# Kernel optimization log

Hardware: AMD Instinct MI355X
Metric: run time of the kernel (lower is better)

Reference implementation:

```python
import jax, jax.numpy as jnp
import numpy as np

NEG_SLOPE = 0.01  # torch leaky_relu default

def _lrelu(x):
    return jax.nn.leaky_relu(x, NEG_SLOPE)

def _l2norm(x, axis):
    # torch F.normalize(p=2, eps=1e-12)
    n = jnp.linalg.norm(x, axis=axis, keepdims=True)
    return x / jnp.maximum(n, 1e-12)

def setup_inputs() -> dict:
    key = jax.random.key(0)
    ks = jax.random.split(key, 12)
    Nda, Nq, C, Din, Dout = 10000, 64, 1024, 128, 256
    target_adj = (jax.random.uniform(ks[0], (Nda, Nda)) < 0.002).astype(jnp.float32)
    query_adj = (jax.random.uniform(ks[1], (Nq, Nq)) < 0.2).astype(jnp.float32)
    node_features_da = jax.random.normal(ks[2], (Nda, Din), dtype=jnp.float32)
    node_features_q = jax.random.normal(ks[3], (Nq, Din), dtype=jnp.float32)
    candidate_set = jax.random.randint(ks[4], (C,), 0, Nda)
    candidate_adj = (jax.random.uniform(ks[5], (C, C)) < 0.01).astype(jnp.float32)
    s_in = 1.0 / np.sqrt(Din).astype(np.float32)
    s_out = 1.0 / np.sqrt(Dout).astype(np.float32)
    W1_da = jax.random.normal(ks[6], (Din, Dout), dtype=jnp.float32) * s_in
    W1_q = jax.random.normal(ks[7], (Din, Dout), dtype=jnp.float32) * s_in
    W2_da = jax.random.normal(ks[8], (Dout, Dout), dtype=jnp.float32) * s_out
    W2_q = jax.random.normal(ks[9], (Dout, Dout), dtype=jnp.float32) * s_out
    threshold = jnp.float32(0.2)
    return {"target_adj": target_adj, "node_features_da": node_features_da,
            "query_adj": query_adj, "node_features_q": node_features_q,
            "candidate_set": candidate_set, "candidate_adj": candidate_adj,
            "threshold": threshold, "W1_da": W1_da, "W1_q": W1_q,
            "W2_da": W2_da, "W2_q": W2_q}

def _cross_cosine(q, da, candidate_set):
    # cosine similarity between each query node and each candidate target node: [Nq, C]
    return _l2norm(q, 1) @ _l2norm(da[candidate_set], 1).T

def reference(target_adj, node_features_da, query_adj, node_features_q,
              candidate_set, candidate_adj, threshold, W1_da, W1_q, W2_da, W2_q):
    # layer 1: GCN propagation on both graphs (gcn(adj,x) = adj @ x @ W)
    da1 = _lrelu(target_adj @ (node_features_da @ W1_da))   # [Nda, D]
    q1 = _lrelu(query_adj @ (node_features_q @ W1_q))       # [Nq, D]
    c1 = _cross_cosine(q1, da1, candidate_set)               # [Nq, C]
    pre_da1 = da1[candidate_set]                             # [C, D]
    # NOTE: da1[candidate_set].data = ... mutates a temporary in torch -> no-op on da1
    att_da1 = _lrelu(da1)                                    # dropout in eval = identity
    h1_q = c1 @ pre_da1                                      # [Nq, D]
    att_q1 = _lrelu(q1 + _l2norm(h1_q, 0))
    # layer 2
    da2 = _lrelu(target_adj @ (att_da1 @ W2_da))
    q2 = _lrelu(query_adj @ (att_q1 @ W2_q))
    c2 = _cross_cosine(q2, da2, candidate_set)
    pre_da2 = da2[candidate_set]
    att_da2 = _lrelu(da2)                                    # in-place update is again a no-op
    h2_q = c2 @ pre_da2
    att_q2 = _lrelu(q2 + _l2norm(h2_q, 0))
    # graph-level matching score per target node
    emb = jnp.mean(att_q2, axis=0, keepdims=True)            # [1, D]
    num = att_da2 @ emb[0]                                   # [Nda]
    den = jnp.maximum(jnp.linalg.norm(att_da2, axis=1) * jnp.linalg.norm(emb), 1e-8)
    end = (num / den)[None, :]                               # [1, Nda]
    # threshold selection expressed with a mask (jit-safe, same math: excluded
    # rows/cols are zero and do not affect L2 norms, sums, or the trace)
    m = (end[0] > threshold).astype(att_da2.dtype)           # [Nda]
    F_ = att_da2 * m[:, None]
    re_adj = F_ @ F_.T                                       # [Nda, Nda]
    nor_re = _l2norm(re_adj, 1) * target_adj                 # elementwise with original adj
    cnt = jnp.sum(m)
    total = jnp.sum(nor_re)
    tr = jnp.trace(nor_re)
    has = cnt > 0
    pre_avg_degree = jnp.where(has, total / jnp.maximum(cnt, 1.0), 0.0)
    pre_avg_nodes = jnp.where(has, tr, 0.0)
    pre_density = jnp.where(has, 2.0 * total / (tr * (tr - 1.0) + 1e-4), 0.0)
    return (end, att_da2, att_q2, pre_avg_degree, pre_density, pre_avg_nodes)
```

## Files before the change

kernel.cpp:

```cpp
#include <hip/hip_runtime.h>

constexpr int NDA = 10000;
constexpr int NQ  = 64;
constexpr int CND = 1024;
constexpr int DIN = 128;
constexpr int D   = 256;
constexpr int CAP = 96;

#define LRELU(x) ((x) >= 0.f ? (x) : 0.01f * (x))

__device__ __forceinline__ float wave_red64(float v) {
#pragma unroll
    for (int o = 32; o; o >>= 1) v += __shfl_down(v, o);
    return v;
}

__global__ __launch_bounds__(256) void build_csr(const float* __restrict__ adj,
                                                 int* __restrict__ cols,
                                                 int* __restrict__ rowcnt) {
    int row = blockIdx.x;
    __shared__ int scnt;
    if (threadIdx.x == 0) scnt = 0;
    __syncthreads();
    const float4* rp = (const float4*)(adj + (size_t)row * NDA);
    for (int i = threadIdx.x; i < NDA / 4; i += 256) {
        float4 v = rp[i];
        if (v.x != 0.f) { int s = atomicAdd(&scnt, 1); if (s < CAP) cols[row * CAP + s] = 4 * i; }
        if (v.y != 0.f) { int s = atomicAdd(&scnt, 1); if (s < CAP) cols[row * CAP + s] = 4 * i + 1; }
        if (v.z != 0.f) { int s = atomicAdd(&scnt, 1); if (s < CAP) cols[row * CAP + s] = 4 * i + 2; }
        if (v.w != 0.f) { int s = atomicAdd(&scnt, 1); if (s < CAP) cols[row * CAP + s] = 4 * i + 3; }
    }
    __syncthreads();
    if (threadIdx.x == 0) rowcnt[row] = min(scnt, CAP);
}

template <int W, bool RELU_IN>
__global__ void spmm(const int* __restrict__ cols,
                     const int* __restrict__ rowcnt,
                     const float* __restrict__ X,
                     float* __restrict__ out) {
    int row = blockIdx.x;
    int d = threadIdx.x;
    int cnt = rowcnt[row];
    __shared__ int sc[CAP];
    if (d < CAP && d < cnt) sc[d] = cols[row * CAP + d];
    __syncthreads();
    float a0 = 0.f, a1 = 0.f, a2 = 0.f, a3 = 0.f;
    int k = 0;
    for (; k + 4 <= cnt; k += 4) {
        float v0 = X[(size_t)sc[k + 0] * W + d];
        float v1 = X[(size_t)sc[k + 1] * W + d];
        float v2 = X[(size_t)sc[k + 2] * W + d];
        float v3 = X[(size_t)sc[k + 3] * W + d];
        if (RELU_IN) { v0 = LRELU(v0); v1 = LRELU(v1); v2 = LRELU(v2); v3 = LRELU(v3); }
        a0 += v0; a1 += v1; a2 += v2; a3 += v3;
    }
    for (; k < cnt; k++) {
        float v = X[(size_t)sc[k] * W + d];
        if (RELU_IN) v = LRELU(v);
        a0 += v;
    }
    out[(size_t)row * W + d] = (a0 + a1) + (a2 + a3);
}

template <bool RELU_C, bool DUAL>
__global__ __launch_bounds__(256) void gemm64(const float* __restrict__ A,
                                              const float* __restrict__ B,
                                              float* __restrict__ C,
                                              float* __restrict__ C2,
                                              int M, int N, int K) {
    __shared__ float As[16][68];
    __shared__ float Bs[16][68];
    const int bm = blockIdx.x * 64;
    const int bn = blockIdx.y * 64;
    const int tid = threadIdx.x;
    const int tx = tid & 15, ty = tid >> 4;
    float acc[4][4] = {};
    for (int k0 = 0; k0 < K; k0 += 16) {
        {
            int m = tid >> 2;
            int k4 = (tid & 3) * 4;
            float4 v = make_float4(0.f, 0.f, 0.f, 0.f);
            if (bm + m < M) v = *(const float4*)(A + (size_t)(bm + m) * K + k0 + k4);
            As[k4 + 0][m] = v.x; As[k4 + 1][m] = v.y; As[k4 + 2][m] = v.z; As[k4 + 3][m] = v.w;
        }
        {
            int kk = tid >> 4;
            int n4 = (tid & 15) * 4;
            float4 v = *(const float4*)(B + (size_t)(k0 + kk) * N + bn + n4);
            Bs[kk][n4 + 0] = v.x; Bs[kk][n4 + 1] = v.y; Bs[kk][n4 + 2] = v.z; Bs[kk][n4 + 3] = v.w;
        }
        __syncthreads();
#pragma unroll
        for (int kk = 0; kk < 16; kk++) {
            float av[4], bv[4];
#pragma unroll
            for (int i = 0; i < 4; i++) av[i] = As[kk][ty * 4 + i];
#pragma unroll
            for (int j = 0; j < 4; j++) bv[j] = Bs[kk][tx * 4 + j];
#pragma unroll
            for (int i = 0; i < 4; i++)
#pragma unroll
                for (int j = 0; j < 4; j++) acc[i][j] += av[i] * bv[j];
        }
        __syncthreads();
    }
#pragma unroll
    for (int i = 0; i < 4; i++) {
        int r = bm + ty * 4 + i;
        if (r < M) {
            float4 v;
            v.x = acc[i][0]; v.y = acc[i][1]; v.z = acc[i][2]; v.w = acc[i][3];
            if (RELU_C) { v.x = LRELU(v.x); v.y = LRELU(v.y); v.z = LRELU(v.z); v.w = LRELU(v.w); }
            *(float4*)(C + (size_t)r * N + bn + tx * 4) = v;
            if (DUAL) {
                float4 u;
                u.x = LRELU(v.x); u.y = LRELU(v.y); u.z = LRELU(v.z); u.w = LRELU(v.w);
                *(float4*)(C2 + (size_t)r * N + bn + tx * 4) = u;
            }
        }
    }
}

__global__ __launch_bounds__(256) void qpath_kernel(const float* __restrict__ Fq,
                                                    const float* __restrict__ Wq,
                                                    const float* __restrict__ Qadj,
                                                    float* __restrict__ q_out,
                                                    float* __restrict__ rnqsq,
                                                    int K) {
    __shared__ float As[16][68];
    __shared__ float Bs[16][68];
    __shared__ float Xs[64][68];
    __shared__ float Qs[64][68];
    __shared__ float sq[64];
    const int bn = blockIdx.x * 64;
    const int tid = threadIdx.x;
    const int tx = tid & 15, ty = tid >> 4;
    float acc[4][4] = {};
    for (int k0 = 0; k0 < K; k0 += 16) {
        {
            int m = tid >> 2;
            int k4 = (tid & 3) * 4;
            float4 v = *(const float4*)(Fq + (size_t)m * K + k0 + k4);
            As[k4 + 0][m] = v.x; As[k4 + 1][m] = v.y; As[k4 + 2][m] = v.z; As[k4 + 3][m] = v.w;
        }
        {
            int kk = tid >> 4;
            int n4 = (tid & 15) * 4;
            float4 v = *(const float4*)(Wq + (size_t)(k0 + kk) * D + bn + n4);
            Bs[kk][n4 + 0] = v.x; Bs[kk][n4 + 1] = v.y; Bs[kk][n4 + 2] = v.z; Bs[kk][n4 + 3] = v.w;
        }
        __syncthreads();
#pragma unroll
        for (int kk = 0; kk < 16; kk++) {
            float av[4], bv[4];
#pragma unroll
            for (int i = 0; i < 4; i++) av[i] = As[kk][ty * 4 + i];
#pragma unroll
            for (int j = 0; j < 4; j++) bv[j] = Bs[kk][tx * 4 + j];
#pragma unroll
            for (int i = 0; i < 4; i++)
#pragma unroll
                for (int j = 0; j < 4; j++) acc[i][j] += av[i] * bv[j];
        }
        __syncthreads();
    }
#pragma unroll
    for (int i = 0; i < 4; i++)
#pragma unroll
        for (int j = 0; j < 4; j++) Xs[ty * 4 + i][tx * 4 + j] = acc[i][j];
    for (int l = tid; l < NQ * NQ; l += 256) Qs[l >> 6][l & 63] = Qadj[l];
    if (tid < 64) sq[tid] = 0.f;
    __syncthreads();
    float a2[4][4] = {};
#pragma unroll 4
    for (int kk = 0; kk < NQ; kk++) {
        float av[4], bv[4];
#pragma unroll
        for (int i = 0; i < 4; i++) av[i] = Qs[ty * 4 + i][kk];
#pragma unroll
        for (int j = 0; j < 4; j++) bv[j] = Xs[kk][tx * 4 + j];
#pragma unroll
        for (int i = 0; i < 4; i++)
#pragma unroll
            for (int j = 0; j < 4; j++) a2[i][j] += av[i] * bv[j];
    }
#pragma unroll
    for (int i = 0; i < 4; i++) {
        float rp = 0.f;
#pragma unroll
        for (int j = 0; j < 4; j++) {
            float v = LRELU(a2[i][j]);
            q_out[(ty * 4 + i) * D + bn + tx * 4 + j] = v;
            rp += v * v;
        }
        atomicAdd(&sq[ty * 4 + i], rp);
    }
    __syncthreads();
    if (tid < 64) atomicAdd(&rnqsq[tid], sq[tid]);
}

__global__ __launch_bounds__(256) void candnorms_kernel(const float* __restrict__ da,
                                                        const int* __restrict__ cand,
                                                        float* __restrict__ rncinv) {
    int b = blockIdx.x;
    const float* src = da + (size_t)cand[b] * D;
    float v = src[threadIdx.x];
    float p = wave_red64(v * v);
    __shared__ float red[4];
    int w = threadIdx.x >> 6, lane = threadIdx.x & 63;
    if (lane == 0) red[w] = p;
    __syncthreads();
    if (threadIdx.x == 0)
        rncinv[b] = 1.f / fmaxf(sqrtf(red[0] + red[1] + red[2] + red[3]), 1e-12f);
}

constexpr int CCH = 128;
__global__ __launch_bounds__(256) void candM_split(const float* __restrict__ da,
                                                   const int* __restrict__ cand,
                                                   const float* __restrict__ rncinv,
                                                   float* __restrict__ M) {
    __shared__ float SA[8][64], SB[8][64];
    const int ti = blockIdx.x, tj = blockIdx.y;
    const int cb = blockIdx.z * CCH;
    const int tid = threadIdx.x;
    const int tx = tid & 15, ty = tid >> 4;
    float acc[4][4] = {};
    for (int c0 = 0; c0 < CCH; c0 += 8) {
        for (int l = tid; l < 512; l += 256) {
            int rr = l >> 6, c = l & 63;
            int cr = cand[cb + c0 + rr];
            float s = rncinv[cb + c0 + rr];
            SA[rr][c] = da[(size_t)cr * D + ti * 64 + c] * s;
            SB[rr][c] = da[(size_t)cr * D + tj * 64 + c];
        }
        __syncthreads();
#pragma unroll
        for (int rr = 0; rr < 8; rr++) {
            float av[4], bv[4];
#pragma unroll
            for (int i = 0; i < 4; i++) av[i] = SA[rr][ty * 4 + i];
#pragma unroll
            for (int j = 0; j < 4; j++) bv[j] = SB[rr][tx * 4 + j];
#pragma unroll
            for (int i = 0; i < 4; i++)
#pragma unroll
                for (int j = 0; j < 4; j++) acc[i][j] += av[i] * bv[j];
        }
        __syncthreads();
    }
#pragma unroll
    for (int i = 0; i < 4; i++)
#pragma unroll
        for (int j = 0; j < 4; j++)
            atomicAdd(&M[(ti * 64 + ty * 4 + i) * D + tj * 64 + tx * 4 + j], acc[i][j]);
}

__global__ __launch_bounds__(256) void hq_gemm(const float* __restrict__ q,
                                               const float* __restrict__ rnqsq,
                                               float* __restrict__ M,
                                               float* __restrict__ h) {
    __shared__ float As[16][68];
    __shared__ float Bs[16][68];
    const int bn = blockIdx.x * 64;
    const int tid = threadIdx.x;
    const int tx = tid & 15, ty = tid >> 4;
    float acc[4][4] = {};
    const float4 z4 = make_float4(0.f, 0.f, 0.f, 0.f);
    for (int k0 = 0; k0 < D; k0 += 16) {
        {
            int m = tid >> 2;
            int k4 = (tid & 3) * 4;
            float s = 1.f / fmaxf(sqrtf(rnqsq[m]), 1e-12f);
            float4 v = *(const float4*)(q + (size_t)m * D + k0 + k4);
            As[k4 + 0][m] = v.x * s; As[k4 + 1][m] = v.y * s;
            As[k4 + 2][m] = v.z * s; As[k4 + 3][m] = v.w * s;
        }
        {
            int kk = tid >> 4;
            int n4 = (tid & 15) * 4;
            float4 v = *(const float4*)(M + (size_t)(k0 + kk) * D + bn + n4);
            *(float4*)(M + (size_t)(k0 + kk) * D + bn + n4) = z4;
            Bs[kk][n4 + 0] = v.x; Bs[kk][n4 + 1] = v.y; Bs[kk][n4 + 2] = v.z; Bs[kk][n4 + 3] = v.w;
        }
        __syncthreads();
#pragma unroll
        for (int kk = 0; kk < 16; kk++) {
            float av[4], bv[4];
#pragma unroll
            for (int i = 0; i < 4; i++) av[i] = As[kk][ty * 4 + i];
#pragma unroll
            for (int j = 0; j < 4; j++) bv[j] = Bs[kk][tx * 4 + j];
#pragma unroll
            for (int i = 0; i < 4; i++)
#pragma unroll
                for (int j = 0; j < 4; j++) acc[i][j] += av[i] * bv[j];
        }
        __syncthreads();
    }
#pragma unroll
    for (int i = 0; i < 4; i++)
#pragma unroll
        for (int j = 0; j < 4; j++)
            h[(ty * 4 + i) * D + bn + tx * 4 + j] = acc[i][j];
}

__global__ __launch_bounds__(256) void attq_kernel(const float* __restrict__ q,
                                                   const float* __restrict__ h,
                                                   float* __restrict__ attq,
                                                   float* __restrict__ emb,
                                                   float* __restrict__ rnqsq) {
    int d = threadIdx.x;
    if (d < 64) rnqsq[d] = 0.f;
    float hv[NQ];
    float ss = 0.f;
#pragma unroll
    for (int r = 0; r < NQ; r++) {
        hv[r] = h[r * D + d];
        ss += hv[r] * hv[r];
    }
    float inv = 1.f / fmaxf(sqrtf(ss), 1e-12f);
    float es = 0.f;
#pragma unroll
    for (int r = 0; r < NQ; r++) {
        float v = q[r * D + d] + hv[r] * inv;
        v = LRELU(v);
        attq[r * D + d] = v;
        es += v;
    }
    if (emb) {
        float e = es * (1.f / (float)NQ);
        emb[d] = e;
        float p = wave_red64(e * e);
        __shared__ float red[4];
        int w = d >> 6, lane = d & 63;
        if (lane == 0) red[w] = p;
        __syncthreads();
        if (d == 0) emb[D] = sqrtf(red[0] + red[1] + red[2] + red[3]);
    }
}

__global__ __launch_bounds__(256) void end_kernel(const float* __restrict__ A,
                                                  const float* __restrict__ emb,
                                                  const float* __restrict__ thr_p,
                                                  float* __restrict__ endv,
                                                  float* __restrict__ m,
                                                  float* __restrict__ cnt) {
    __shared__ float se[D];
    __shared__ float scnt;
    int d = threadIdx.x;
    se[d] = emb[d];
    if (d == 0) scnt = 0.f;
    __syncthreads();
    float embn = emb[D];
    float thr = *thr_p;
    int w = d >> 6, lane = d & 63;
    int row = blockIdx.x * 4 + w;
    const float* ar = A + (size_t)row * D;
    float num = 0.f, sq = 0.f;
#pragma unroll
    for (int s = 0; s < 4; s++) {
        float v = ar[lane + 64 * s];
        num += v * se[lane + 64 * s];
        sq += v * v;
    }
#pragma unroll
    for (int o = 32; o; o >>= 1) { num += __shfl_down(num, o); sq += __shfl_down(sq, o); }
    if (lane == 0) {
        float den = fmaxf(sqrtf(sq) * embn, 1e-8f);
        float e = num / den;
        endv[row] = e;
        float mv = e > thr ? 1.f : 0.f;
        m[row] = mv;
        if (mv != 0.f) atomicAdd(&scnt, 1.f);
    }
    __syncthreads();
    if (d == 0 && scnt != 0.f) atomicAdd(cnt, scnt);
}

constexpr int GCHUNK = 1000;
__global__ __launch_bounds__(256) void G_kernel(const float* __restrict__ A,
                                                const float* __restrict__ m,
                                                float* __restrict__ G) {
    __shared__ float SA[8][64], SB[8][64];
    int ti = blockIdx.x >> 2, tj = blockIdx.x & 3;
    int base = blockIdx.y * GCHUNK;
    int tid = threadIdx.x;
    int tx = tid & 15, ty = tid >> 4;
    float acc[4][4] = {};
    for (int g0 = 0; g0 < GCHUNK; g0 += 8) {
        for (int l = tid; l < 512; l += 256) {
            int rr = l >> 6, c = l & 63;
            int r = base + g0 + rr;
            float mv = m[r];
            SA[rr][c] = A[(size_t)r * D + ti * 64 + c] * mv;
            SB[rr][c] = A[(size_t)r * D + tj * 64 + c];
        }
        __syncthreads();
#pragma unroll
        for (int rr = 0; rr < 8; rr++) {
            float av[4], bv[4];
#pragma unroll
            for (int i = 0; i < 4; i++) av[i] = SA[rr][ty * 4 + i];
#pragma unroll
            for (int j = 0; j < 4; j++) bv[j] = SB[rr][tx * 4 + j];
#pragma unroll
            for (int i = 0; i < 4; i++)
#pragma unroll
                for (int j = 0; j < 4; j++) acc[i][j] += av[i] * bv[j];
        }
        __syncthreads();
    }
#pragma unroll
    for (int i = 0; i < 4; i++)
#pragma unroll
        for (int j = 0; j < 4; j++)
            atomicAdd(&G[(ti * 64 + ty * 4 + i) * D + tj * 64 + tx * 4 + j], acc[i][j]);
}

__global__ __launch_bounds__(256) void final_kernel(const int* __restrict__ cols,
                                                    const int* __restrict__ rowcnt,
                                                    const float* __restrict__ m,
                                                    const float* __restrict__ A,
                                                    const float* __restrict__ H,
                                                    double* __restrict__ total,
                                                    double* __restrict__ tr) {
    int i = blockIdx.x;
    if (m[i] == 0.f) return;
    __shared__ float sa[D];
    __shared__ int sc[CAP];
    __shared__ float red[4], red2[4];
    __shared__ float sdenom;
    int d = threadIdx.x;
    float av = A[(size_t)i * D + d];
    sa[d] = av;
    int cnt = rowcnt[i];
    if (d < cnt) sc[d] = cols[i * CAP + d];
    float p = wave_red64(av * H[(size_t)i * D + d]);
    int w = d >> 6, lane = d & 63;
    if (lane == 0) red[w] = p;
    __syncthreads();
    if (d == 0) sdenom = fmaxf(sqrtf(red[0] + red[1] + red[2] + red[3]), 1e-12f);
    __syncthreads();
    float accs = 0.f, acct = 0.f;
    for (int k = w; k < cnt; k += 4) {
        int j = sc[k];
        if (m[j] != 0.f) {
            const float* aj = A + (size_t)j * D;
            float t = sa[lane] * aj[lane] + sa[lane + 64] * aj[lane + 64]
                    + sa[lane + 128] * aj[lane + 128] + sa[lane + 192] * aj[lane + 192];
            t = wave_red64(t);
            if (lane == 0) { accs += t; if (j == i) acct += t; }
        }
    }
    if (lane == 0) { red[w] = accs; red2[w] = acct; }
    __syncthreads();
    if (d == 0) {
        float s = red[0] + red[1] + red[2] + red[3];
        float t2 = red2[0] + red2[1] + red2[2] + red2[3];
        double inv = 1.0 / (double)sdenom;
        if (s != 0.f) atomicAdd(total, (double)s * inv);
        if (t2 != 0.f) atomicAdd(tr, (double)t2 * inv);
    }
}

__global__ void scalars_kernel(const float* __restrict__ cnt,
                               const double* __restrict__ total,
                               const double* __restrict__ tr,
                               float* __restrict__ out) {
    float c = *cnt;
    float T = (float)*total;
    float R = (float)*tr;
    bool has = c > 0.f;
    out[0] = has ? (T / fmaxf(c, 1.f)) : 0.f;
    out[1] = has ? (2.f * T / (R * (R - 1.f) + 1e-4f)) : 0.f;
    out[2] = has ? R : 0.f;
}

extern "C" void kernel_launch(void* const* d_in, const int* in_sizes, int n_in,
                              void* d_out, int out_size, void* d_ws, size_t ws_size,
                              hipStream_t stream) {
    (void)in_sizes; (void)n_in; (void)out_size; (void)ws_size;
    const float* adj  = (const float*)d_in[0];
    const float* Fda  = (const float*)d_in[1];
    const float* Qadj = (const float*)d_in[2];
    const float* Fq   = (const float*)d_in[3];
    const int*   cand = (const int*)d_in[4];
    const float* thr  = (const float*)d_in[6];
    const float* W1da = (const float*)d_in[7];
    const float* W1q  = (const float*)d_in[8];
    const float* W2da = (const float*)d_in[9];
    const float* W2q  = (const float*)d_in[10];

    float* out = (float*)d_out;
    float* o_end    = out;
    float* o_attda2 = out + NDA;
    float* o_attq2  = out + NDA + (size_t)NDA * D;
    float* o_sc     = o_attq2 + NQ * D;

    char* w = (char*)d_ws;
    size_t off = 0;
    auto alloc = [&](size_t b) { size_t r = off; off += (b + 255) & ~(size_t)255; return r; };
    float* bufA = (float*)(w + alloc((size_t)NDA * D * 4));
    float* bufB = (float*)(w + alloc((size_t)NDA * D * 4));
    float* bufC = (float*)(w + alloc((size_t)NDA * D * 4));
    int* colsb   = (int*)(w + alloc((size_t)NDA * CAP * 4));
    int* rowcntb = (int*)(w + alloc((size_t)NDA * 4));
    float* mbuf  = (float*)(w + alloc((size_t)NDA * 4));
    char* zbase = w + alloc(525000);
    float* Gb     = (float*)zbase;
    float* Mb     = (float*)(zbase + 262144);
    float* rnqsqb = (float*)(zbase + 524288);
    float* cntb   = (float*)(zbase + 524544);
    double* totb  = (double*)(zbase + 524552);
    double* trb   = (double*)(zbase + 524560);
    float* q1b  = (float*)(w + alloc((size_t)NQ * D * 4));
    float* aq1  = (float*)(w + alloc((size_t)NQ * D * 4));
    float* q2b  = (float*)(w + alloc((size_t)NQ * D * 4));
    float* hb   = (float*)(w + alloc((size_t)NQ * D * 4));
    float* rncinv = (float*)(w + alloc((size_t)CND * 4));
    float* embb   = (float*)(w + alloc((size_t)(D + 1) * 4));

    hipMemsetAsync(zbase, 0, 524576, stream);

    const dim3 gBig((NDA + 63) / 64, D / 64);

    build_csr<<<NDA, 256, 0, stream>>>(adj, colsb, rowcntb);
    qpath_kernel<<<D / 64, 256, 0, stream>>>(Fq, W1q, Qadj, q1b, rnqsqb, DIN);
    spmm<DIN, false><<<NDA, DIN, 0, stream>>>(colsb, rowcntb, Fda, bufA);
    gemm64<true, false><<<gBig, 256, 0, stream>>>(bufA, W1da, bufB, nullptr, NDA, D, DIN);
    candnorms_kernel<<<CND, 256, 0, stream>>>(bufB, cand, rncinv);
    candM_split<<<dim3(4, 4, CND / CCH), 256, 0, stream>>>(bufB, cand, rncinv, Mb);
    hq_gemm<<<D / 64, 256, 0, stream>>>(q1b, rnqsqb, Mb, hb);
    attq_kernel<<<1, 256, 0, stream>>>(q1b, hb, aq1, nullptr, rnqsqb);
    qpath_kernel<<<D / 64, 256, 0, stream>>>(aq1, W2q, Qadj, q2b, rnqsqb, D);
    spmm<D, true><<<NDA, D, 0, stream>>>(colsb, rowcntb, bufB, bufA);
    gemm64<true, true><<<gBig, 256, 0, stream>>>(bufA, W2da, bufC, o_attda2, NDA, D, D);
    candnorms_kernel<<<CND, 256, 0, stream>>>(bufC, cand, rncinv);
    candM_split<<<dim3(4, 4, CND / CCH), 256, 0, stream>>>(bufC, cand, rncinv, Mb);
    hq_gemm<<<D / 64, 256, 0, stream>>>(q2b, rnqsqb, Mb, hb);
    attq_kernel<<<1, 256, 0, stream>>>(q2b, hb, o_attq2, embb, rnqsqb);
    end_kernel<<<NDA / 4, 256, 0, stream>>>(o_attda2, embb, thr, o_end, mbuf, cntb);
    G_kernel<<<dim3(16, NDA / GCHUNK), 256, 0, stream>>>(o_attda2, mbuf, Gb);
    gemm64<false, false><<<gBig, 256, 0, stream>>>(o_attda2, Gb, bufB, nullptr, NDA, D, D);
    final_kernel<<<NDA, 256, 0, stream>>>(colsb, rowcntb, mbuf, o_attda2, bufB, totb, trb);
    scalars_kernel<<<1, 1, 0, stream>>>(cntb, totb, trb, o_sc);
}
```

Before: 1.080 ms.

## Fuse row norms into GEMM epilogue, merge hq/attq, gather bf16 activations in SpMM

Row squared norms are now accumulated with atomics in the GEMM epilogue, which replaces the separate candidate-norm kernels. The hq GEMM and attq kernels are merged into one multi-block kernel, and the embedding-norm computation moves into end_kernel. The first-layer activated output is also written in bf16, so the second SpMM gathers half the bytes. The cost is extra atomics per row and reduced precision in the layer-2 input, which could move results past tolerance.

```diff
diff --git a/kernel.cpp b/kernel.cpp
--- a/kernel.cpp
+++ b/kernel.cpp
@@ -1,4 +1,5 @@
 #include <hip/hip_runtime.h>
+#include <hip/hip_bf16.h>
 
 constexpr int NDA = 10000;
 constexpr int NQ  = 64;
@@ -8,6 +9,8 @@
 constexpr int CAP = 96;
 
 #define LRELU(x) ((x) >= 0.f ? (x) : 0.01f * (x))
+
+struct alignas(8) bf4 { __hip_bfloat16 a, b, c, d; };
 
 __device__ __forceinline__ float wave_red64(float v) {
 #pragma unroll
@@ -34,11 +37,11 @@
     if (threadIdx.x == 0) rowcnt[row] = min(scnt, CAP);
 }
 
-template <int W, bool RELU_IN>
-__global__ void spmm(const int* __restrict__ cols,
-                     const int* __restrict__ rowcnt,
-                     const float* __restrict__ X,
-                     float* __restrict__ out) {
+template <int W>
+__global__ void spmm_f32(const int* __restrict__ cols,
+                         const int* __restrict__ rowcnt,
+                         const float* __restrict__ X,
+                         float* __restrict__ out) {
     int row = blockIdx.x;
     int d = threadIdx.x;
     int cnt = rowcnt[row];
@@ -48,26 +51,44 @@
     float a0 = 0.f, a1 = 0.f, a2 = 0.f, a3 = 0.f;
     int k = 0;
     for (; k + 4 <= cnt; k += 4) {
-        float v0 = X[(size_t)sc[k + 0] * W + d];
-        float v1 = X[(size_t)sc[k + 1] * W + d];
-        float v2 = X[(size_t)sc[k + 2] * W + d];
-        float v3 = X[(size_t)sc[k + 3] * W + d];
-        if (RELU_IN) { v0 = LRELU(v0); v1 = LRELU(v1); v2 = LRELU(v2); v3 = LRELU(v3); }
-        a0 += v0; a1 += v1; a2 += v2; a3 += v3;
-    }
-    for (; k < cnt; k++) {
-        float v = X[(size_t)sc[k] * W + d];
-        if (RELU_IN) v = LRELU(v);
-        a0 += v;
-    }
+        a0 += X[(size_t)sc[k + 0] * W + d];
+        a1 += X[(size_t)sc[k + 1] * W + d];
+        a2 += X[(size_t)sc[k + 2] * W + d];
+        a3 += X[(size_t)sc[k + 3] * W + d];
+    }
+    for (; k < cnt; k++) a0 += X[(size_t)sc[k] * W + d];
     out[(size_t)row * W + d] = (a0 + a1) + (a2 + a3);
 }
 
-template <bool RELU_C, bool DUAL>
+__global__ void spmm_bf16(const int* __restrict__ cols,
+                          const int* __restrict__ rowcnt,
+                          const __hip_bfloat16* __restrict__ X,
+                          float* __restrict__ out) {
+    int row = blockIdx.x;
+    int d = threadIdx.x;
+    int cnt = rowcnt[row];
+    __shared__ int sc[CAP];
+    if (d < CAP && d < cnt) sc[d] = cols[row * CAP + d];
+    __syncthreads();
+    float a0 = 0.f, a1 = 0.f, a2 = 0.f, a3 = 0.f;
+    int k = 0;
+    for (; k + 4 <= cnt; k += 4) {
+        a0 += __bfloat162float(X[(size_t)sc[k + 0] * D + d]);
+        a1 += __bfloat162float(X[(size_t)sc[k + 1] * D + d]);
+        a2 += __bfloat162float(X[(size_t)sc[k + 2] * D + d]);
+        a3 += __bfloat162float(X[(size_t)sc[k + 3] * D + d]);
+    }
+    for (; k < cnt; k++) a0 += __bfloat162float(X[(size_t)sc[k] * D + d]);
+    out[(size_t)row * D + d] = (a0 + a1) + (a2 + a3);
+}
+
+template <bool RELU_C, bool DUAL, bool BF16OUT>
 __global__ __launch_bounds__(256) void gemm64(const float* __restrict__ A,
                                               const float* __restrict__ B,
                                               float* __restrict__ C,
                                               float* __restrict__ C2,
+                                              __hip_bfloat16* __restrict__ bfout,
+                                              float* __restrict__ rowsq,
                                               int M, int N, int K) {
     __shared__ float As[16][68];
     __shared__ float Bs[16][68];
@@ -113,10 +134,22 @@
             v.x = acc[i][0]; v.y = acc[i][1]; v.z = acc[i][2]; v.w = acc[i][3];
             if (RELU_C) { v.x = LRELU(v.x); v.y = LRELU(v.y); v.z = LRELU(v.z); v.w = LRELU(v.w); }
             *(float4*)(C + (size_t)r * N + bn + tx * 4) = v;
+            if (rowsq) {
+                float rp = v.x * v.x + v.y * v.y + v.z * v.z + v.w * v.w;
+                atomicAdd(&rowsq[r], rp);
+            }
             if (DUAL) {
                 float4 u;
                 u.x = LRELU(v.x); u.y = LRELU(v.y); u.z = LRELU(v.z); u.w = LRELU(v.w);
                 *(float4*)(C2 + (size_t)r * N + bn + tx * 4) = u;
+            }
+            if (BF16OUT) {
+                bf4 t;
+                t.a = __float2bfloat16(LRELU(v.x));
+                t.b = __float2bfloat16(LRELU(v.y));
+                t.c = __float2bfloat16(LRELU(v.z));
+                t.d = __float2bfloat16(LRELU(v.w));
+                *(bf4*)(bfout + (size_t)r * N + bn + tx * 4) = t;
             }
         }
     }
@@ -200,25 +233,10 @@
     if (tid < 64) atomicAdd(&rnqsq[tid], sq[tid]);
 }
 
-__global__ __launch_bounds__(256) void candnorms_kernel(const float* __restrict__ da,
-                                                        const int* __restrict__ cand,
-                                                        float* __restrict__ rncinv) {
-    int b = blockIdx.x;
-    const float* src = da + (size_t)cand[b] * D;
-    float v = src[threadIdx.x];
-    float p = wave_red64(v * v);
-    __shared__ float red[4];
-    int w = threadIdx.x >> 6, lane = threadIdx.x & 63;
-    if (lane == 0) red[w] = p;
-    __syncthreads();
-    if (threadIdx.x == 0)
-        rncinv[b] = 1.f / fmaxf(sqrtf(red[0] + red[1] + red[2] + red[3]), 1e-12f);
-}
-
 constexpr int CCH = 128;
 __global__ __launch_bounds__(256) void candM_split(const float* __restrict__ da,
                                                    const int* __restrict__ cand,
-                                                   const float* __restrict__ rncinv,
+                                                   const float* __restrict__ rowsq,
                                                    float* __restrict__ M) {
     __shared__ float SA[8][64], SB[8][64];
     const int ti = blockIdx.x, tj = blockIdx.y;
@@ -230,7 +248,7 @@
         for (int l = tid; l < 512; l += 256) {
             int rr = l >> 6, c = l & 63;
             int cr = cand[cb + c0 + rr];
-            float s = rncinv[cb + c0 + rr];
+            float s = 1.f / fmaxf(sqrtf(rowsq[cr]), 1e-12f);
             SA[rr][c] = da[(size_t)cr * D + ti * 64 + c] * s;
             SB[rr][c] = da[(size_t)cr * D + tj * 64 + c];
         }
@@ -256,25 +274,29 @@
             atomicAdd(&M[(ti * 64 + ty * 4 + i) * D + tj * 64 + tx * 4 + j], acc[i][j]);
 }
 
-__global__ __launch_bounds__(256) void hq_gemm(const float* __restrict__ q,
-                                               const float* __restrict__ rnqsq,
-                                               float* __restrict__ M,
-                                               float* __restrict__ h) {
+template <bool EMB>
+__global__ __launch_bounds__(256) void hq_attq_kernel(const float* __restrict__ q,
+                                                      const float* __restrict__ rnqsq,
+                                                      float* __restrict__ M,
+                                                      float* __restrict__ attq,
+                                                      float* __restrict__ emb) {
     __shared__ float As[16][68];
     __shared__ float Bs[16][68];
+    __shared__ float cred[16][64];
+    __shared__ float sinv[64];
     const int bn = blockIdx.x * 64;
     const int tid = threadIdx.x;
     const int tx = tid & 15, ty = tid >> 4;
+    const int am = tid >> 2;
+    const float ascale = 1.f / fmaxf(sqrtf(rnqsq[am]), 1e-12f);
     float acc[4][4] = {};
     const float4 z4 = make_float4(0.f, 0.f, 0.f, 0.f);
     for (int k0 = 0; k0 < D; k0 += 16) {
         {
-            int m = tid >> 2;
             int k4 = (tid & 3) * 4;
-            float s = 1.f / fmaxf(sqrtf(rnqsq[m]), 1e-12f);
-            float4 v = *(const float4*)(q + (size_t)m * D + k0 + k4);
-            As[k4 + 0][m] = v.x * s; As[k4 + 1][m] = v.y * s;
-            As[k4 + 2][m] = v.z * s; As[k4 + 3][m] = v.w * s;
+            float4 v = *(const float4*)(q + (size_t)am * D + k0 + k4);
+            As[k4 + 0][am] = v.x * ascale; As[k4 + 1][am] = v.y * ascale;
+            As[k4 + 2][am] = v.z * ascale; As[k4 + 3][am] = v.w * ascale;
         }
         {
             int kk = tid >> 4;
@@ -299,44 +321,44 @@
         __syncthreads();
     }
 #pragma unroll
-    for (int i = 0; i < 4; i++)
-#pragma unroll
-        for (int j = 0; j < 4; j++)
-            h[(ty * 4 + i) * D + bn + tx * 4 + j] = acc[i][j];
-}
-
-__global__ __launch_bounds__(256) void attq_kernel(const float* __restrict__ q,
-                                                   const float* __restrict__ h,
-                                                   float* __restrict__ attq,
-                                                   float* __restrict__ emb,
-                                                   float* __restrict__ rnqsq) {
-    int d = threadIdx.x;
-    if (d < 64) rnqsq[d] = 0.f;
-    float hv[NQ];
-    float ss = 0.f;
-#pragma unroll
-    for (int r = 0; r < NQ; r++) {
-        hv[r] = h[r * D + d];
-        ss += hv[r] * hv[r];
-    }
-    float inv = 1.f / fmaxf(sqrtf(ss), 1e-12f);
-    float es = 0.f;
-#pragma unroll
-    for (int r = 0; r < NQ; r++) {
-        float v = q[r * D + d] + hv[r] * inv;
-        v = LRELU(v);
-        attq[r * D + d] = v;
-        es += v;
-    }
-    if (emb) {
-        float e = es * (1.f / (float)NQ);
-        emb[d] = e;
-        float p = wave_red64(e * e);
-        __shared__ float red[4];
-        int w = d >> 6, lane = d & 63;
-        if (lane == 0) red[w] = p;
-        __syncthreads();
-        if (d == 0) emb[D] = sqrtf(red[0] + red[1] + red[2] + red[3]);
+    for (int j = 0; j < 4; j++) {
+        float p = 0.f;
+#pragma unroll
+        for (int i = 0; i < 4; i++) p += acc[i][j] * acc[i][j];
+        cred[ty][tx * 4 + j] = p;
+    }
+    __syncthreads();
+    if (tid < 64) {
+        float s = 0.f;
+#pragma unroll
+        for (int t = 0; t < 16; t++) s += cred[t][tid];
+        sinv[tid] = 1.f / fmaxf(sqrtf(s), 1e-12f);
+    }
+    __syncthreads();
+    float esum[4] = {};
+#pragma unroll
+    for (int i = 0; i < 4; i++) {
+        int r = ty * 4 + i;
+        float4 q4 = *(const float4*)(q + (size_t)r * D + bn + tx * 4);
+        float4 v;
+        v.x = LRELU(q4.x + acc[i][0] * sinv[tx * 4 + 0]);
+        v.y = LRELU(q4.y + acc[i][1] * sinv[tx * 4 + 1]);
+        v.z = LRELU(q4.z + acc[i][2] * sinv[tx * 4 + 2]);
+        v.w = LRELU(q4.w + acc[i][3] * sinv[tx * 4 + 3]);
+        *(float4*)(attq + (size_t)r * D + bn + tx * 4) = v;
+        if (EMB) { esum[0] += v.x; esum[1] += v.y; esum[2] += v.z; esum[3] += v.w; }
+    }
+    if (EMB) {
+        __syncthreads();
+#pragma unroll
+        for (int j = 0; j < 4; j++) cred[ty][tx * 4 + j] = esum[j];
+        __syncthreads();
+        if (tid < 64) {
+            float s = 0.f;
+#pragma unroll
+            for (int t = 0; t < 16; t++) s += cred[t][tid];
+            emb[bn + tid] = s * (1.f / (float)NQ);
+        }
     }
 }
 
@@ -347,14 +369,22 @@
                                                   float* __restrict__ m,
                                                   float* __restrict__ cnt) {
     __shared__ float se[D];
-    __shared__ float scnt;
+    __shared__ float red[4];
+    __shared__ float scnt, sembn;
     int d = threadIdx.x;
     se[d] = emb[d];
     if (d == 0) scnt = 0.f;
     __syncthreads();
-    float embn = emb[D];
+    int w = d >> 6, lane = d & 63;
+    {
+        float p = wave_red64(se[d] * se[d]);
+        if (lane == 0) red[w] = p;
+    }
+    __syncthreads();
+    if (d == 0) sembn = sqrtf(red[0] + red[1] + red[2] + red[3]);
+    __syncthreads();
+    float embn = sembn;
     float thr = *thr_p;
-    int w = d >> 6, lane = d & 63;
     int row = blockIdx.x * 4 + w;
     const float* ar = A + (size_t)row * D;
     float num = 0.f, sq = 0.f;
@@ -504,45 +534,47 @@
     float* bufA = (float*)(w + alloc((size_t)NDA * D * 4));
     float* bufB = (float*)(w + alloc((size_t)NDA * D * 4));
     float* bufC = (float*)(w + alloc((size_t)NDA * D * 4));
+    __hip_bfloat16* attda1_bf = (__hip_bfloat16*)(w + alloc((size_t)NDA * D * 2));
     int* colsb   = (int*)(w + alloc((size_t)NDA * CAP * 4));
     int* rowcntb = (int*)(w + alloc((size_t)NDA * 4));
     float* mbuf  = (float*)(w + alloc((size_t)NDA * 4));
-    char* zbase = w + alloc(525000);
-    float* Gb     = (float*)zbase;
-    float* Mb     = (float*)(zbase + 262144);
-    float* rnqsqb = (float*)(zbase + 524288);
-    float* cntb   = (float*)(zbase + 524544);
-    double* totb  = (double*)(zbase + 524552);
-    double* trb   = (double*)(zbase + 524560);
+    size_t zsz = 262144 * 2 + 40000 * 4 * 2 + 256 * 2 + 64;
+    char* zbase = w + alloc(zsz);
+    float* Gb      = (float*)zbase;
+    float* Mb      = (float*)(zbase + 262144);
+    float* rsq1    = (float*)(zbase + 524288);
+    float* rsq2    = (float*)(zbase + 524288 + 160000);
+    float* rnqsq1  = (float*)(zbase + 524288 + 320000);
+    float* rnqsq2  = (float*)(zbase + 524288 + 320256);
+    float* cntb    = (float*)(zbase + 524288 + 320512);
+    double* totb   = (double*)(zbase + 524288 + 320520);
+    double* trb    = (double*)(zbase + 524288 + 320528);
     float* q1b  = (float*)(w + alloc((size_t)NQ * D * 4));
     float* aq1  = (float*)(w + alloc((size_t)NQ * D * 4));
     float* q2b  = (float*)(w + alloc((size_t)NQ * D * 4));
-    float* hb   = (float*)(w + alloc((size_t)NQ * D * 4));
-    float* rncinv = (float*)(w + alloc((size_t)CND * 4));
-    float* embb   = (float*)(w + alloc((size_t)(D + 1) * 4));
-
-    hipMemsetAsync(zbase, 0, 524576, stream);
+    float* embb = (float*)(w + alloc((size_t)D * 4));
+
+    hipMemsetAsync(zbase, 0, zsz, stream);
 
     const dim3 gBig((NDA + 63) / 64, D / 64);
 
     build_csr<<<NDA, 256, 0, stream>>>(adj, colsb, rowcntb);
-    qpath_kernel<<<D / 64, 256, 0, stream>>>(Fq, W1q, Qadj, q1b, rnqsqb, DIN);
-    spmm<DIN, false><<<NDA, DIN, 0, stream>>>(colsb, rowcntb, Fda, bufA);
-    gemm64<true, false><<<gBig, 256, 0, stream>>>(bufA, W1da, bufB, nullptr, NDA, D, DIN);
-    candnorms_kernel<<<CND, 256, 0, stream>>>(bufB, cand, rncinv);
-    candM_split<<<dim3(4, 4, CND / CCH), 256, 0, stream>>>(bufB, cand, rncinv, Mb);
-    hq_gemm<<<D / 64, 256, 0, stream>>>(q1b, rnqsqb, Mb, hb);
-    attq_kernel<<<1, 256, 0, stream>>>(q1b, hb, aq1, nullptr, rnqsqb);
-    qpath_kernel<<<D / 64, 256, 0, stream>>>(aq1, W2q, Qadj, q2b, rnqsqb, D);
-    spmm<D, true><<<NDA, D, 0, stream>>>(colsb, rowcntb, bufB, bufA);
-    gemm64<true, true><<<gBig, 256, 0, stream>>>(bufA, W2da, bufC, o_attda2, NDA, D, D);
-    candnorms_kernel<<<CND, 256, 0, stream>>>(bufC, cand, rncinv);
-    candM_split<<<dim3(4, 4, CND / CCH), 256, 0, stream>>>(bufC, cand, rncinv, Mb);
-    hq_gemm<<<D / 64, 256, 0, stream>>>(q2b, rnqsqb, Mb, hb);
-    attq_kernel<<<1, 256, 0, stream>>>(q2b, hb, o_attq2, embb, rnqsqb);
+    qpath_kernel<<<D / 64, 256, 0, stream>>>(Fq, W1q, Qadj, q1b, rnqsq1, DIN);
+    spmm_f32<DIN><<<NDA, DIN, 0, stream>>>(colsb, rowcntb, Fda, bufA);
+    gemm64<true, false, true><<<gBig, 256, 0, stream>>>(bufA, W1da, bufB, nullptr,
+                                                        attda1_bf, rsq1, NDA, D, DIN);
+    candM_split<<<dim3(4, 4, CND / CCH), 256, 0, stream>>>(bufB, cand, rsq1, Mb);
+    hq_attq_kernel<false><<<D / 64, 256, 0, stream>>>(q1b, rnqsq1, Mb, aq1, nullptr);
+    qpath_kernel<<<D / 64, 256, 0, stream>>>(aq1, W2q, Qadj, q2b, rnqsq2, D);
+    spmm_bf16<<<NDA, D, 0, stream>>>(colsb, rowcntb, attda1_bf, bufA);
+    gemm64<true, true, false><<<gBig, 256, 0, stream>>>(bufA, W2da, bufC, o_attda2,
+                                                        nullptr, rsq2, NDA, D, D);
+    candM_split<<<dim3(4, 4, CND / CCH), 256, 0, stream>>>(bufC, cand, rsq2, Mb);
+    hq_attq_kernel<true><<<D / 64, 256, 0, stream>>>(q2b, rnqsq2, Mb, o_attq2, embb);
     end_kernel<<<NDA / 4, 256, 0, stream>>>(o_attda2, embb, thr, o_end, mbuf, cntb);
     G_kernel<<<dim3(16, NDA / GCHUNK), 256, 0, stream>>>(o_attda2, mbuf, Gb);
-    gemm64<false, false><<<gBig, 256, 0, stream>>>(o_attda2, Gb, bufB, nullptr, NDA, D, D);
+    gemm64<false, false, false><<<gBig, 256, 0, stream>>>(o_attda2, Gb, bufB, nullptr,
+                                                          nullptr, nullptr, NDA, D, D);
     final_kernel<<<NDA, 256, 0, stream>>>(colsb, rowcntb, mbuf, o_attda2, bufB, totb, trb);
     scalars_kernel<<<1, 1, 0, stream>>>(cntb, totb, trb, o_sc);
 }
```

Result: slower. 1.158 ms (+7.2%).
